# Kernel tuning notes

Measured on AMD Instinct MI355X. Metric: run time of the kernel, lower is better.

Reference implementation:

```python
import jax, jax.numpy as jnp
import numpy as np

K_ORDER = 3
GRID_N = 10
GRID_LO, GRID_HI = -2.0, 2.0
LAYERS = [(49, 256), (256, 256), (256, 10)]
NCOEF = GRID_N + K_ORDER  # 13


def mish(x):
    return x * jnp.tanh(jax.nn.softplus(x))


def bspline_basis(x):
    # x: (B, in) -> basis (B, in, GRID_N + K_ORDER)
    h = (GRID_HI - GRID_LO) / GRID_N
    knots = GRID_LO + h * jnp.arange(-K_ORDER, GRID_N + K_ORDER + 1, dtype=x.dtype)  # (G+2k+1,)
    xx = x[..., None]
    B = ((xx >= knots[:-1]) & (xx < knots[1:])).astype(x.dtype)  # degree-0, (B,in,G+2k)
    for d in range(1, K_ORDER + 1):
        left = (xx - knots[: -(d + 1)]) / (knots[d:-1] - knots[: -(d + 1)]) * B[..., :-1]
        right = (knots[d + 1:] - xx) / (knots[d + 1:] - knots[1:-d]) * B[..., 1:]
        B = left + right
    return B  # (B, in, G+k)


def kan_layer(x, coef, scale_base, scale_sp, bias):
    # x: (B,in); coef: (in,out,G+k); scales: (in,out); bias: (out,)
    basis = bspline_basis(x)                                   # (B,in,G+k)
    spline = jnp.einsum('big,iog->bo', basis, coef * scale_sp[..., None])
    base = jnp.einsum('bi,io->bo', mish(x), scale_base)
    return base + spline + bias


def setup_inputs() -> dict:
    key = jax.random.key(0)
    ks = jax.random.split(key, 1 + 4 * len(LAYERS))
    inp = {'x': jax.random.normal(ks[0], (8192, 1, 28, 28), dtype=jnp.float32)}
    i = 1
    for li, (fin, fout) in enumerate(LAYERS, start=1):
        inp[f'coef{li}'] = 0.1 * jax.random.normal(ks[i], (fin, fout, NCOEF), dtype=jnp.float32); i += 1
        inp[f'sb{li}'] = 1.0 + 0.1 * jax.random.normal(ks[i], (fin, fout), dtype=jnp.float32); i += 1
        inp[f'sp{li}'] = 1.0 + 0.1 * jax.random.normal(ks[i], (fin, fout), dtype=jnp.float32); i += 1
        inp[f'b{li}'] = jnp.zeros((fout,), dtype=jnp.float32); i += 1
    return inp


def reference(x, coef1, sb1, sp1, b1, coef2, sb2, sp2, b2, coef3, sb3, sp3, b3):
    B = x.shape[0]
    # avg_pool2d(x, 4): 28x28 -> 7x7
    h = x.reshape(B, 1, 7, 4, 7, 4).mean(axis=(3, 5))
    h = h.reshape(B, 49)
    h = kan_layer(h, coef1, sb1, sp1, b1)
    h = kan_layer(h, coef2, sb2, sp2, b2)
    h = kan_layer(h, coef3, sb3, sp3, b3)
    return jax.nn.log_softmax(h, axis=1)
```

## Files before the change

### kernel.cpp

```cpp
#include <hip/hip_runtime.h>
#include <hip/hip_bf16.h>

typedef __bf16 bf16x8_t __attribute__((ext_vector_type(8)));
typedef float f32x4_t __attribute__((ext_vector_type(4)));
using bf16 = __hip_bfloat16;

#define ASG __attribute__((address_space(1)))
#define ASL __attribute__((address_space(3)))

__device__ __forceinline__ void gld_lds16(const void* g, void* l) {
  __builtin_amdgcn_global_load_lds((ASG void*)const_cast<void*>(g),
                                   (ASL void*)l, 16, 0, 0);
}

__device__ __forceinline__ unsigned short f2bf_bits(float v) {
  __hip_bfloat16 h = __float2bfloat16(v);
  return *reinterpret_cast<unsigned short*>(&h);
}

__device__ __forceinline__ float mish_f(float x) {
  float z = __expf(x);
  float n = z * (z + 2.0f);
  float m = x * n / (n + 2.0f);
  return (x > 10.0f) ? x : m;
}

__device__ __forceinline__ void kan_feats28(bf16* dst, float x) {
  unsigned int* d32 = (unsigned int*)dst;
#pragma unroll
  for (int d = 0; d < 7; ++d) d32[d] = 0u;
  float t = (x + 3.2f) * 2.5f;
  if (t >= 0.0f && t < 16.0f) {
    float tf = floorf(t);
    int c = (int)tf;
    float u = t - tf;
    float um = 1.0f - u;
    float u2 = u * u, u3 = u2 * u;
    const float s6 = 1.0f / 6.0f;
    float w0 = um * um * um * s6;
    float w1 = (3.0f * u3 - 6.0f * u2 + 4.0f) * s6;
    float w2 = (-3.0f * u3 + 3.0f * u2 + 3.0f * u + 1.0f) * s6;
    float w3 = u3 * s6;
    int j0 = c - 3;
    if (j0 >= 0)               dst[j0]     = __float2bfloat16(w0);
    if (j0 >= -1 && j0 <= 11)  dst[j0 + 1] = __float2bfloat16(w1);
    if (j0 >= -2 && j0 <= 10)  dst[j0 + 2] = __float2bfloat16(w2);
    if (j0 <= 9)               dst[j0 + 3] = __float2bfloat16(w3);
  }
  dst[13] = __float2bfloat16(mish_f(x));
}

__global__ __launch_bounds__(256) void prep_all(
    const float* __restrict__ c1, const float* __restrict__ sb1, const float* __restrict__ sp1,
    const float* __restrict__ c2, const float* __restrict__ sb2, const float* __restrict__ sp2,
    const float* __restrict__ c3, const float* __restrict__ sb3, const float* __restrict__ sp3,
    bf16* __restrict__ W1t, bf16* __restrict__ W2f, bf16* __restrict__ W3t) {
  const int b = blockIdx.x, o = threadIdx.x;
  float vals[14];
  if (b < 49) {
    const int i = b;
    const size_t io = (size_t)i * 256 + o;
    const float spv = sp1[io];
#pragma unroll
    for (int r = 0; r < 13; ++r) vals[r] = c1[io * 13 + r] * spv;
    vals[13] = sb1[io];
    unsigned int* dst = (unsigned int*)(W1t + (size_t)o * 704 + i * 14);
#pragma unroll
    for (int d = 0; d < 7; ++d)
      dst[d] = (unsigned int)f2bf_bits(vals[2 * d]) |
               ((unsigned int)f2bf_bits(vals[2 * d + 1]) << 16);
  } else if (b == 49) {
    unsigned int* dst = (unsigned int*)(W1t + (size_t)o * 704 + 686);
#pragma unroll
    for (int d = 0; d < 9; ++d) dst[d] = 0u;
  } else if (b < 306) {
    const int i = b - 50;
    const size_t io = (size_t)i * 256 + o;
    const float spv = sp2[io];
#pragma unroll
    for (int r = 0; r < 13; ++r) vals[r] = c2[io * 13 + r] * spv;
    vals[13] = sb2[io];
    const int ntg = o >> 4, lr = o & 15;
#pragma unroll
    for (int d = 0; d < 7; ++d) {
      const int k2 = i * 14 + 2 * d;
      const int kc = k2 / 224, rem = k2 % 224;
      const int ks = rem / 32, r2 = rem % 32, quad = r2 / 8, el = r2 % 8;
      const size_t off = ((size_t)((kc * 7 + ks) * 16 + ntg)) * 512 + lr * 32 + quad * 8 + el;
      *(unsigned int*)(W2f + off) = (unsigned int)f2bf_bits(vals[2 * d]) |
                                    ((unsigned int)f2bf_bits(vals[2 * d + 1]) << 16);
    }
  } else {
    const int i = b - 306;
    if (o < 10) {
      const size_t io = (size_t)i * 10 + o;
      const float spv = sp3[io];
#pragma unroll
      for (int r = 0; r < 13; ++r) vals[r] = c3[io * 13 + r] * spv;
      vals[13] = sb3[io];
      unsigned int* dst = (unsigned int*)(W3t + (size_t)o * 3584 + i * 14);
#pragma unroll
      for (int d = 0; d < 7; ++d)
        dst[d] = (unsigned int)f2bf_bits(vals[2 * d]) |
                 ((unsigned int)f2bf_bits(vals[2 * d + 1]) << 16);
    } else if (o < 16) {
      unsigned int* dst = (unsigned int*)(W3t + (size_t)o * 3584 + i * 14);
#pragma unroll
      for (int d = 0; d < 7; ++d) dst[d] = 0u;
    }
  }
}

__global__ __launch_bounds__(256) void pool_basis1(const float* __restrict__ x,
                                                   bf16* __restrict__ A1) {
  __shared__ __align__(16) float xs[784];
  __shared__ __align__(16) bf16 arow[704];
  const int b = blockIdx.x, t = threadIdx.x;
  if (t < 196) *(float4*)(&xs[t * 4]) = *(const float4*)(x + (size_t)b * 784 + t * 4);
  __syncthreads();
  if (t < 49) {
    const int oh = t / 7, ow = t % 7;
    float s = 0.f;
#pragma unroll
    for (int r = 0; r < 4; ++r)
#pragma unroll
      for (int c = 0; c < 4; ++c) s += xs[(oh * 4 + r) * 28 + ow * 4 + c];
    kan_feats28(&arow[t * 14], s * (1.0f / 16.0f));
  } else if (t < 67) {
    arow[686 + (t - 49)] = __float2bfloat16(0.0f);
  }
  __syncthreads();
  if (t < 88) ((uint4*)((char*)A1 + (size_t)b * 1408))[t] = ((const uint4*)arow)[t];
}

__global__ __launch_bounds__(256) void gemm1s(
    const bf16* __restrict__ A, const bf16* __restrict__ Wt,
    const float* __restrict__ bias, float* __restrict__ H) {
  constexpr int K = 704;
  __shared__ __align__(16) bf16 As[64 * 64];
  __shared__ __align__(16) bf16 Bs[64 * 64];
  const int t = threadIdx.x;
  const int wv = t >> 6, lane = t & 63, quad = lane >> 4, lr = lane & 15;
  const int n0 = blockIdx.x * 64;
  const int m0 = blockIdx.y * 64;
  const int srow0 = lane >> 3;
  const int cg = (lane & 7) ^ srow0;
  const bf16* gA0 = A + (size_t)(m0 + 8 * wv + srow0) * K + cg * 8;
  const bf16* gA1 = A + (size_t)(m0 + 32 + 8 * wv + srow0) * K + cg * 8;
  const bf16* gB0 = Wt + (size_t)(n0 + 8 * wv + srow0) * K + cg * 8;
  const bf16* gB1 = Wt + (size_t)(n0 + 32 + 8 * wv + srow0) * K + cg * 8;
  char* const lA = (char*)As + wv * 1024;
  char* const lB = (char*)Bs + wv * 1024;
  const int wm = (wv & 1) * 32, wn = (wv >> 1) * 32;
  const int swz = lr & 7;
  f32x4_t acc00 = {0.f, 0.f, 0.f, 0.f}, acc01 = acc00, acc10 = acc00, acc11 = acc00;
  for (int k0 = 0; k0 < K; k0 += 64) {
    gld_lds16(gA0 + k0, lA);
    gld_lds16(gA1 + k0, lA + 4096);
    gld_lds16(gB0 + k0, lB);
    gld_lds16(gB1 + k0, lB + 4096);
    __syncthreads();
#pragma unroll
    for (int s = 0; s < 2; ++s) {
      const int co = ((s * 4 + quad) ^ swz) * 16;
      bf16x8_t a0 = *(const bf16x8_t*)((char*)As + (wm + lr) * 128 + co);
      bf16x8_t a1 = *(const bf16x8_t*)((char*)As + (wm + 16 + lr) * 128 + co);
      bf16x8_t b0 = *(const bf16x8_t*)((char*)Bs + (wn + lr) * 128 + co);
      bf16x8_t b1 = *(const bf16x8_t*)((char*)Bs + (wn + 16 + lr) * 128 + co);
      acc00 = __builtin_amdgcn_mfma_f32_16x16x32_bf16(a0, b0, acc00, 0, 0, 0);
      acc01 = __builtin_amdgcn_mfma_f32_16x16x32_bf16(a0, b1, acc01, 0, 0, 0);
      acc10 = __builtin_amdgcn_mfma_f32_16x16x32_bf16(a1, b0, acc10, 0, 0, 0);
      acc11 = __builtin_amdgcn_mfma_f32_16x16x32_bf16(a1, b1, acc11, 0, 0, 0);
    }
    __syncthreads();
  }
  const int cb = n0 + wn + lr;
  const float bn0 = bias[cb], bn1 = bias[cb + 16];
#pragma unroll
  for (int r = 0; r < 4; ++r) {
    const size_t row = (size_t)(m0 + wm + quad * 4 + r);
    H[row * 256 + cb] = acc00[r] + bn0;
    H[row * 256 + cb + 16] = acc01[r] + bn1;
    H[(row + 16) * 256 + cb] = acc10[r] + bn0;
    H[(row + 16) * 256 + cb + 16] = acc11[r] + bn1;
  }
}

__global__ __launch_bounds__(256, 2) void kan_gemm2(
    const float* __restrict__ Hin, const bf16* __restrict__ W2f,
    float* __restrict__ Hp) {
  __shared__ __align__(16) bf16 As[2][64 * 232];
  const int t = threadIdx.x;
  const int w = t >> 6, lane = t & 63, quad = lane >> 4, lr = lane & 15;
  const int m0 = blockIdx.x * 64;
  const int z = blockIdx.y;
  const int ej = t & 15, er0 = t >> 4;
  const int foff = lr * 32 + quad * 8;
  f32x4_t acc[4][4];
#pragma unroll
  for (int m = 0; m < 4; ++m)
#pragma unroll
    for (int n = 0; n < 4; ++n) acc[m][n] = (f32x4_t){0.f, 0.f, 0.f, 0.f};
  const float* hp = Hin + (size_t)(m0 + er0) * 256 + z * 64 + ej;
#pragma unroll
  for (int e = 0; e < 4; ++e)
    kan_feats28(As[0] + (er0 + 16 * e) * 232 + ej * 14, hp[e * 16 * 256]);
  for (int kcl = 0; kcl < 4; ++kcl) {
    __syncthreads();
    const bf16* cur = As[kcl & 1];
    bf16* nxt = As[(kcl & 1) ^ 1];
    const int kc = z * 4 + kcl;
#pragma unroll
    for (int ks = 0; ks < 7; ++ks) {
      const size_t fb = ((size_t)((kc * 7 + ks) * 16 + w * 4)) * 512 + foff;
      bf16x8_t b0 = *(const bf16x8_t*)(W2f + fb);
      bf16x8_t b1 = *(const bf16x8_t*)(W2f + fb + 512);
      bf16x8_t b2 = *(const bf16x8_t*)(W2f + fb + 1024);
      bf16x8_t b3 = *(const bf16x8_t*)(W2f + fb + 1536);
#pragma unroll
      for (int m = 0; m < 4; ++m) {
        bf16x8_t a = *(const bf16x8_t*)(cur + (m * 16 + lr) * 232 + ks * 32 + quad * 8);
        acc[m][0] = __builtin_amdgcn_mfma_f32_16x16x32_bf16(a, b0, acc[m][0], 0, 0, 0);
        acc[m][1] = __builtin_amdgcn_mfma_f32_16x16x32_bf16(a, b1, acc[m][1], 0, 0, 0);
        acc[m][2] = __builtin_amdgcn_mfma_f32_16x16x32_bf16(a, b2, acc[m][2], 0, 0, 0);
        acc[m][3] = __builtin_amdgcn_mfma_f32_16x16x32_bf16(a, b3, acc[m][3], 0, 0, 0);
      }
    }
    if (kcl < 3) {
#pragma unroll
      for (int e = 0; e < 4; ++e)
        kan_feats28(nxt + (er0 + 16 * e) * 232 + ej * 14,
                    hp[e * 16 * 256 + (kcl + 1) * 16]);
    }
  }
  float* Hpz = Hp + (size_t)z * (8192 * 256);
  const int c0 = w * 64 + lr;
#pragma unroll
  for (int m = 0; m < 4; ++m)
#pragma unroll
    for (int r = 0; r < 4; ++r) {
      const size_t row = (size_t)(m0 + m * 16 + quad * 4 + r);
#pragma unroll
      for (int n = 0; n < 4; ++n)
        Hpz[row * 256 + c0 + n * 16] = acc[m][n][r];
    }
}

__global__ __launch_bounds__(256) void kan_gemm3(
    const float* __restrict__ Hp, const float* __restrict__ b2,
    const bf16* __restrict__ Wt, float* __restrict__ part) {
  constexpr int K = 3584;
  __shared__ __align__(16) bf16 As[64 * 232];
  __shared__ __align__(16) bf16 Bs[16 * 256];
  const int t = threadIdx.x;
  const int wv = t >> 6, lane = t & 63, quad = lane >> 4, lr = lane & 15;
  const int m0 = blockIdx.x * 64;
  const int z = blockIdx.y;
  const int ej = t & 15, er0 = t >> 4;
  const int brow_sub = lane >> 5, bslot = lane & 31;
  f32x4_t acc = {0.f, 0.f, 0.f, 0.f};
  for (int kcl = 0; kcl < 4; ++kcl) {
    const int kc = z * 4 + kcl;
#pragma unroll
    for (int n = 0; n < 2; ++n) {
      const int row = wv * 4 + n * 2 + brow_sub;
      int c = bslot ^ (row & 7);
      if (c >= 28) c = 0;
      const bf16* src = Wt + (size_t)row * K + kc * 224 + c * 8;
      gld_lds16(src, (char*)Bs + (wv * 4 + n * 2) * 512);
    }
    const float bc = b2[kc * 16 + ej];
    const float* hp = Hp + (size_t)(m0 + er0) * 256 + kc * 16 + ej;
    bf16* arow = As + er0 * 232 + ej * 14;
#pragma unroll
    for (int e = 0; e < 4; ++e) {
      const size_t idx = (size_t)e * 16 * 256;
      float h = hp[idx] + hp[idx + 2097152] + hp[idx + 4194304] + hp[idx + 6291456] + bc;
      kan_feats28(arow + e * 16 * 232, h);
    }
    __syncthreads();
#pragma unroll
    for (int ks = 0; ks < 7; ++ks) {
      const int coA = ks * 64 + quad * 16;
      const int sb = ((ks * 4 + quad) ^ (lr & 7)) * 16;
      bf16x8_t a = *(const bf16x8_t*)((const char*)As + (wv * 16 + lr) * 464 + coA);
      bf16x8_t b = *(const bf16x8_t*)((const char*)Bs + lr * 512 + sb);
      acc = __builtin_amdgcn_mfma_f32_16x16x32_bf16(a, b, acc, 0, 0, 0);
    }
    __syncthreads();
  }
#pragma unroll
  for (int r = 0; r < 4; ++r)
    part[(size_t)z * 131072 + (size_t)lr * 8192 + (m0 + wv * 16 + quad * 4 + r)] = acc[r];
}

__global__ __launch_bounds__(256) void lsm(const float* __restrict__ part,
                                           const float* __restrict__ b3,
                                           float* __restrict__ out) {
  const int row = blockIdx.x * 256 + threadIdx.x;
  float v[10];
#pragma unroll
  for (int o = 0; o < 10; ++o) {
    float s = b3[o];
#pragma unroll
    for (int kc = 0; kc < 4; ++kc) s += part[(size_t)kc * 131072 + (size_t)o * 8192 + row];
    v[o] = s;
  }
  float m = v[0];
#pragma unroll
  for (int o = 1; o < 10; ++o) m = fmaxf(m, v[o]);
  float se = 0.f;
#pragma unroll
  for (int o = 0; o < 10; ++o) se += expf(v[o] - m);
  const float l = m + logf(se);
#pragma unroll
  for (int o = 0; o < 10; ++o) out[(size_t)row * 10 + o] = v[o] - l;
}

extern "C" void kernel_launch(void* const* d_in, const int* in_sizes, int n_in,
                              void* d_out, int out_size, void* d_ws, size_t ws_size,
                              hipStream_t stream) {
  const float* x = (const float*)d_in[0];
  const float* coef1 = (const float*)d_in[1];
  const float* sb1 = (const float*)d_in[2];
  const float* sp1 = (const float*)d_in[3];
  const float* b1 = (const float*)d_in[4];
  const float* coef2 = (const float*)d_in[5];
  const float* sb2 = (const float*)d_in[6];
  const float* sp2 = (const float*)d_in[7];
  const float* b2 = (const float*)d_in[8];
  const float* coef3 = (const float*)d_in[9];
  const float* sb3 = (const float*)d_in[10];
  const float* sp3 = (const float*)d_in[11];
  const float* b3 = (const float*)d_in[12];
  float* out = (float*)d_out;

  char* ws = (char*)d_ws;
  size_t off = 0;
  bf16* A1 = (bf16*)(ws + off);    off += 11534336;
  bf16* W1t = (bf16*)(ws + off);   off += 360448;
  bf16* W2f = (bf16*)(ws + off);   off += 1835008;
  bf16* W3t = (bf16*)(ws + off);   off += 114688;
  float* H1 = (float*)(ws + off);  off += 8388608;
  float* Hp = (float*)(ws + off);  off += 33554432;
  float* part = (float*)(ws + off); off += 2097152;

  prep_all<<<562, 256, 0, stream>>>(coef1, sb1, sp1, coef2, sb2, sp2,
                                    coef3, sb3, sp3, W1t, W2f, W3t);
  pool_basis1<<<8192, 256, 0, stream>>>(x, A1);
  gemm1s<<<dim3(4, 128), 256, 0, stream>>>(A1, W1t, b1, H1);
  kan_gemm2<<<dim3(128, 4), 256, 0, stream>>>(H1, W2f, Hp);
  kan_gemm3<<<dim3(128, 4), 256, 0, stream>>>(Hp, b2, W3t, part);
  lsm<<<32, 256, 0, stream>>>(part, b3, out);
}
```

Measured before the change: 151.9 us.

## Batch pooling per block, widen gemm2 to 512 threads with B prefetch, split gemm3 K further

pool_basis1 now handles four images per block, which cuts the block count and widens the loads and stores. kan_gemm2 moves to 512 threads: each wave computes two N tiles instead of four and software-prefetches the B fragments two k-steps ahead. This lowers accumulator register pressure and raises occupancy, so more latency can be hidden. kan_gemm3 splits K across 8 z-slices instead of 4 for more parallelism, which doubles the partial buffer that lsm must reduce.

```diff
diff --git a/kernel.cpp b/kernel.cpp
--- a/kernel.cpp
+++ b/kernel.cpp
@@ -113,24 +113,34 @@
 
 __global__ __launch_bounds__(256) void pool_basis1(const float* __restrict__ x,
                                                    bf16* __restrict__ A1) {
-  __shared__ __align__(16) float xs[784];
-  __shared__ __align__(16) bf16 arow[704];
-  const int b = blockIdx.x, t = threadIdx.x;
-  if (t < 196) *(float4*)(&xs[t * 4]) = *(const float4*)(x + (size_t)b * 784 + t * 4);
+  __shared__ __align__(16) float xs[3136];
+  __shared__ __align__(16) bf16 arow[4 * 704];
+  const int b4 = blockIdx.x * 4, t = threadIdx.x;
+  const float4* xsrc = (const float4*)(x + (size_t)b4 * 784);
+  float4* xd = (float4*)xs;
+#pragma unroll
+  for (int l = t; l < 784; l += 256) xd[l] = xsrc[l];
   __syncthreads();
-  if (t < 49) {
-    const int oh = t / 7, ow = t % 7;
+  if (t < 196) {
+    const int img = t / 49, p = t - img * 49;
+    const int oh = p / 7, ow = p - oh * 7;
+    const float* xi = xs + img * 784;
     float s = 0.f;
 #pragma unroll
     for (int r = 0; r < 4; ++r)
 #pragma unroll
-      for (int c = 0; c < 4; ++c) s += xs[(oh * 4 + r) * 28 + ow * 4 + c];
-    kan_feats28(&arow[t * 14], s * (1.0f / 16.0f));
-  } else if (t < 67) {
-    arow[686 + (t - 49)] = __float2bfloat16(0.0f);
+      for (int c = 0; c < 4; ++c) s += xi[(oh * 4 + r) * 28 + ow * 4 + c];
+    kan_feats28(&arow[img * 704 + p * 14], s * (1.0f / 16.0f));
+  } else if (t < 232) {
+    const int q = t - 196;
+    const int img = q / 9, d = q - img * 9;
+    ((unsigned int*)(arow + img * 704 + 686))[d] = 0u;
   }
   __syncthreads();
-  if (t < 88) ((uint4*)((char*)A1 + (size_t)b * 1408))[t] = ((const uint4*)arow)[t];
+  uint4* dst = (uint4*)(A1 + (size_t)b4 * 704);
+  const uint4* src = (const uint4*)arow;
+#pragma unroll
+  for (int l = t; l < 352; l += 256) dst[l] = src[l];
 }
 
 __global__ __launch_bounds__(256) void gemm1s(
@@ -186,7 +196,7 @@
   }
 }
 
-__global__ __launch_bounds__(256, 2) void kan_gemm2(
+__global__ __launch_bounds__(512, 4) void kan_gemm2(
     const float* __restrict__ Hin, const bf16* __restrict__ W2f,
     float* __restrict__ Hp) {
   __shared__ __align__(16) bf16 As[2][64 * 232];
@@ -194,55 +204,60 @@
   const int w = t >> 6, lane = t & 63, quad = lane >> 4, lr = lane & 15;
   const int m0 = blockIdx.x * 64;
   const int z = blockIdx.y;
-  const int ej = t & 15, er0 = t >> 4;
+  const int ej = t & 15, er0 = (t >> 4) & 31;
   const int foff = lr * 32 + quad * 8;
-  f32x4_t acc[4][4];
-#pragma unroll
-  for (int m = 0; m < 4; ++m)
-#pragma unroll
-    for (int n = 0; n < 4; ++n) acc[m][n] = (f32x4_t){0.f, 0.f, 0.f, 0.f};
+  f32x4_t acc[4][2];
+#pragma unroll
+  for (int m = 0; m < 4; ++m) {
+    acc[m][0] = (f32x4_t){0.f, 0.f, 0.f, 0.f};
+    acc[m][1] = (f32x4_t){0.f, 0.f, 0.f, 0.f};
+  }
   const float* hp = Hin + (size_t)(m0 + er0) * 256 + z * 64 + ej;
-#pragma unroll
-  for (int e = 0; e < 4; ++e)
-    kan_feats28(As[0] + (er0 + 16 * e) * 232 + ej * 14, hp[e * 16 * 256]);
+  kan_feats28(As[0] + er0 * 232 + ej * 14, hp[0]);
+  kan_feats28(As[0] + (er0 + 32) * 232 + ej * 14, hp[32 * 256]);
+  size_t fb = ((size_t)(z * 28 * 16 + w * 2)) * 512 + foff;
+  bf16x8_t bA0 = *(const bf16x8_t*)(W2f + fb);
+  bf16x8_t bA1 = *(const bf16x8_t*)(W2f + fb + 512);
+  bf16x8_t bB0 = *(const bf16x8_t*)(W2f + fb + 8192);
+  bf16x8_t bB1 = *(const bf16x8_t*)(W2f + fb + 8192 + 512);
+  fb += 2 * 8192;
+#pragma unroll
   for (int kcl = 0; kcl < 4; ++kcl) {
     __syncthreads();
     const bf16* cur = As[kcl & 1];
     bf16* nxt = As[(kcl & 1) ^ 1];
-    const int kc = z * 4 + kcl;
 #pragma unroll
     for (int ks = 0; ks < 7; ++ks) {
-      const size_t fb = ((size_t)((kc * 7 + ks) * 16 + w * 4)) * 512 + foff;
-      bf16x8_t b0 = *(const bf16x8_t*)(W2f + fb);
-      bf16x8_t b1 = *(const bf16x8_t*)(W2f + fb + 512);
-      bf16x8_t b2 = *(const bf16x8_t*)(W2f + fb + 1024);
-      bf16x8_t b3 = *(const bf16x8_t*)(W2f + fb + 1536);
+      bf16x8_t bN0, bN1;
+      if (kcl * 7 + ks < 26) {
+        bN0 = *(const bf16x8_t*)(W2f + fb);
+        bN1 = *(const bf16x8_t*)(W2f + fb + 512);
+      } else {
+        bN0 = bB0; bN1 = bB1;
+      }
 #pragma unroll
       for (int m = 0; m < 4; ++m) {
         bf16x8_t a = *(const bf16x8_t*)(cur + (m * 16 + lr) * 232 + ks * 32 + quad * 8);
-        acc[m][0] = __builtin_amdgcn_mfma_f32_16x16x32_bf16(a, b0, acc[m][0], 0, 0, 0);
-        acc[m][1] = __builtin_amdgcn_mfma_f32_16x16x32_bf16(a, b1, acc[m][1], 0, 0, 0);
-        acc[m][2] = __builtin_amdgcn_mfma_f32_16x16x32_bf16(a, b2, acc[m][2], 0, 0, 0);
-        acc[m][3] = __builtin_amdgcn_mfma_f32_16x16x32_bf16(a, b3, acc[m][3], 0, 0, 0);
+        acc[m][0] = __builtin_amdgcn_mfma_f32_16x16x32_bf16(a, bA0, acc[m][0], 0, 0, 0);
+        acc[m][1] = __builtin_amdgcn_mfma_f32_16x16x32_bf16(a, bA1, acc[m][1], 0, 0, 0);
       }
+      bA0 = bB0; bA1 = bB1; bB0 = bN0; bB1 = bN1;
+      fb += 8192;
     }
     if (kcl < 3) {
-#pragma unroll
-      for (int e = 0; e < 4; ++e)
-        kan_feats28(nxt + (er0 + 16 * e) * 232 + ej * 14,
-                    hp[e * 16 * 256 + (kcl + 1) * 16]);
+      kan_feats28(nxt + er0 * 232 + ej * 14, hp[(kcl + 1) * 16]);
+      kan_feats28(nxt + (er0 + 32) * 232 + ej * 14, hp[32 * 256 + (kcl + 1) * 16]);
     }
   }
   float* Hpz = Hp + (size_t)z * (8192 * 256);
-  const int c0 = w * 64 + lr;
+  const int c0 = w * 32 + lr;
 #pragma unroll
   for (int m = 0; m < 4; ++m)
 #pragma unroll
     for (int r = 0; r < 4; ++r) {
       const size_t row = (size_t)(m0 + m * 16 + quad * 4 + r);
-#pragma unroll
-      for (int n = 0; n < 4; ++n)
-        Hpz[row * 256 + c0 + n * 16] = acc[m][n][r];
+      Hpz[row * 256 + c0] = acc[m][0][r];
+      Hpz[row * 256 + c0 + 16] = acc[m][1][r];
     }
 }
 
@@ -259,8 +274,8 @@
   const int ej = t & 15, er0 = t >> 4;
   const int brow_sub = lane >> 5, bslot = lane & 31;
   f32x4_t acc = {0.f, 0.f, 0.f, 0.f};
-  for (int kcl = 0; kcl < 4; ++kcl) {
-    const int kc = z * 4 + kcl;
+  for (int kcl = 0; kcl < 2; ++kcl) {
+    const int kc = z * 2 + kcl;
 #pragma unroll
     for (int n = 0; n < 2; ++n) {
       const int row = wv * 4 + n * 2 + brow_sub;
@@ -303,7 +318,7 @@
   for (int o = 0; o < 10; ++o) {
     float s = b3[o];
 #pragma unroll
-    for (int kc = 0; kc < 4; ++kc) s += part[(size_t)kc * 131072 + (size_t)o * 8192 + row];
+    for (int kc = 0; kc < 8; ++kc) s += part[(size_t)kc * 131072 + (size_t)o * 8192 + row];
     v[o] = s;
   }
   float m = v[0];
@@ -343,13 +358,13 @@
   bf16* W3t = (bf16*)(ws + off);   off += 114688;
   float* H1 = (float*)(ws + off);  off += 8388608;
   float* Hp = (float*)(ws + off);  off += 33554432;
-  float* part = (float*)(ws + off); off += 2097152;
+  float* part = (float*)(ws + off); off += 4194304;
 
   prep_all<<<562, 256, 0, stream>>>(coef1, sb1, sp1, coef2, sb2, sp2,
                                     coef3, sb3, sp3, W1t, W2f, W3t);
-  pool_basis1<<<8192, 256, 0, stream>>>(x, A1);
+  pool_basis1<<<2048, 256, 0, stream>>>(x, A1);
   gemm1s<<<dim3(4, 128), 256, 0, stream>>>(A1, W1t, b1, H1);
-  kan_gemm2<<<dim3(128, 4), 256, 0, stream>>>(H1, W2f, Hp);
-  kan_gemm3<<<dim3(128, 4), 256, 0, stream>>>(Hp, b2, W3t, part);
+  kan_gemm2<<<dim3(128, 4), 512, 0, stream>>>(H1, W2f, Hp);
+  kan_gemm3<<<dim3(128, 8), 256, 0, stream>>>(Hp, b2, W3t, part);
   lsm<<<32, 256, 0, stream>>>(part, b3, out);
 }
```

Result: faster. 146.2 us (-3.8%).
